# Optimization experiments

Measured on AMD Instinct MI355X. Metric: run time of the kernel, lower is better.

Reference implementation:

```python
import jax, jax.numpy as jnp
import numpy as np

KERNEL_MUL = 2.0
KERNEL_NUM = 5
FIX_SIGMA = None


def setup_inputs() -> dict:
    key = jax.random.key(0)
    k1, k2 = jax.random.split(key)
    source = jax.random.normal(k1, (4096, 512), dtype=jnp.float32)
    target = jax.random.normal(k2, (4096, 512), dtype=jnp.float32)
    return {"source": source, "target": target}


def reference(source, target):
    batch_size = source.shape[0]
    total = jnp.concatenate([source, target], axis=0)  # [N, D], N = n1 + n2
    n_samples = total.shape[0]

    # Pairwise squared L2 distances via Gram-matrix trick (same math as
    # the explicit NxNxD broadcast in the original, without materializing it).
    sq = jnp.sum(total * total, axis=1)               # [N]
    gram = total @ total.T                            # [N, N]
    l2 = sq[:, None] + sq[None, :] - 2.0 * gram       # [N, N]

    if FIX_SIGMA:
        bandwidth = jnp.asarray(FIX_SIGMA, dtype=l2.dtype)
    else:
        # torch used L2_distance.data -> no gradient through bandwidth
        bandwidth = jax.lax.stop_gradient(jnp.sum(l2)) / (n_samples ** 2 - n_samples)
    bandwidth = bandwidth / (KERNEL_MUL ** (KERNEL_NUM // 2))

    # Multi-bandwidth Gaussian kernel sum
    kernels = jnp.zeros_like(l2)
    for i in range(KERNEL_NUM):
        kernels = kernels + jnp.exp(-l2 / (bandwidth * (KERNEL_MUL ** i)))

    b = batch_size
    XX = kernels[:b, :b]
    YY = kernels[b:, b:]
    XY = kernels[:b, b:]
    YX = kernels[b:, :b]
    loss = jnp.mean(XX + YY - XY - YX)
    return loss
```

## Files before the change

### kernel.cpp

```cpp
#include <hip/hip_runtime.h>
#include <math.h>

typedef float f32x4 __attribute__((ext_vector_type(4)));
typedef int   i32x4 __attribute__((ext_vector_type(4)));
typedef signed char i8x8 __attribute__((ext_vector_type(8)));

#define NROWS 8192
#define NCOLS 512
#define BHALF 4096
#define NT    64
#define NBLK  2080
#define CSPART 256
#define QS    24.0f
#define INV_S2 (1.0f / (24.0f * 24.0f))

__global__ void k_conv(const float* __restrict__ src, const float* __restrict__ tgt,
                       signed char* __restrict__ bfrag, float* __restrict__ sq,
                       int* __restrict__ sqi, float* __restrict__ cspart) {
    __shared__ signed char ldsc[32][528];
    __shared__ float colp[4][NCOLS];
    int t = threadIdx.x, w = t >> 6, l = t & 63;
    int r0 = blockIdx.x * 32;
    float c0x=0.f,c0y=0.f,c0z=0.f,c0w=0.f, c1x=0.f,c1y=0.f,c1z=0.f,c1w=0.f;
    #pragma unroll
    for (int r = 0; r < 8; ++r) {
        int row = r0 + w * 8 + r;
        const float* base = (row < BHALF) ? (src + (size_t)row * NCOLS)
                                          : (tgt + (size_t)(row - BHALF) * NCOLS);
        float4 a = ((const float4*)base)[2 * l];
        float4 b = ((const float4*)base)[2 * l + 1];
        int q0 = (int)rintf(fminf(fmaxf(a.x * QS, -127.f), 127.f));
        int q1 = (int)rintf(fminf(fmaxf(a.y * QS, -127.f), 127.f));
        int q2 = (int)rintf(fminf(fmaxf(a.z * QS, -127.f), 127.f));
        int q3 = (int)rintf(fminf(fmaxf(a.w * QS, -127.f), 127.f));
        int q4 = (int)rintf(fminf(fmaxf(b.x * QS, -127.f), 127.f));
        int q5 = (int)rintf(fminf(fmaxf(b.y * QS, -127.f), 127.f));
        int q6 = (int)rintf(fminf(fmaxf(b.z * QS, -127.f), 127.f));
        int q7 = (int)rintf(fminf(fmaxf(b.w * QS, -127.f), 127.f));
        i8x8 v8;
        v8[0]=(signed char)q0; v8[1]=(signed char)q1; v8[2]=(signed char)q2; v8[3]=(signed char)q3;
        v8[4]=(signed char)q4; v8[5]=(signed char)q5; v8[6]=(signed char)q6; v8[7]=(signed char)q7;
        *(i8x8*)&ldsc[w * 8 + r][l * 8] = v8;
        float s = a.x*a.x + a.y*a.y + a.z*a.z + a.w*a.w
                + b.x*b.x + b.y*b.y + b.z*b.z + b.w*b.w;
        int si = q0*q0 + q1*q1 + q2*q2 + q3*q3 + q4*q4 + q5*q5 + q6*q6 + q7*q7;
        #pragma unroll
        for (int o = 32; o > 0; o >>= 1) {
            s  += __shfl_down(s, o);
            si += __shfl_down(si, o);
        }
        if (l == 0) { sq[row] = s; sqi[row] = si; }
        c0x += a.x; c0y += a.y; c0z += a.z; c0w += a.w;
        c1x += b.x; c1y += b.y; c1z += b.z; c1w += b.w;
    }
    colp[w][l*8+0] = c0x; colp[w][l*8+1] = c0y; colp[w][l*8+2] = c0z; colp[w][l*8+3] = c0w;
    colp[w][l*8+4] = c1x; colp[w][l*8+5] = c1y; colp[w][l*8+6] = c1z; colp[w][l*8+7] = c1w;
    __syncthreads();
    float s0 = colp[0][t] + colp[1][t] + colp[2][t] + colp[3][t];
    float s1 = colp[0][t+256] + colp[1][t+256] + colp[2][t+256] + colp[3][t+256];
    cspart[(size_t)blockIdx.x * NCOLS + t]       = s0;
    cspart[(size_t)blockIdx.x * NCOLS + t + 256] = s1;
    int rg0 = blockIdx.x * 2;
    #pragma unroll
    for (int c4 = 0; c4 < 4; ++c4) {
        int c = c4 * 256 + t;
        int g = c >> 9, sl = (c >> 4) & 31, lrr = c & 15;
        i32x4 v = *(const i32x4*)&ldsc[g * 16 + lrr][sl * 16];
        *(i32x4*)(bfrag + (size_t)(rg0 + g) * 8192 + sl * 256 + lrr * 16) = v;
    }
}

__global__ void k_bw(const float* __restrict__ sq, const float* __restrict__ cspart,
                     float* __restrict__ cvals) {
    __shared__ double red[1024];
    int t = threadIdx.x;
    double a = 0.0;
    #pragma unroll
    for (int i = 0; i < 8; ++i) a += (double)sq[t + i * 1024];
    red[t] = a; __syncthreads();
    for (int o = 512; o > 0; o >>= 1) { if (t < o) red[t] += red[t + o]; __syncthreads(); }
    double sT = red[0];
    __syncthreads();
    int c = t & 511, h = t >> 9;
    double d0 = 0.0, d1 = 0.0, d2 = 0.0, d3 = 0.0;
    int p0 = h * 128;
    #pragma unroll 8
    for (int p = 0; p < 128; p += 4) {
        d0 += (double)cspart[(size_t)(p0 + p + 0) * NCOLS + c];
        d1 += (double)cspart[(size_t)(p0 + p + 1) * NCOLS + c];
        d2 += (double)cspart[(size_t)(p0 + p + 2) * NCOLS + c];
        d3 += (double)cspart[(size_t)(p0 + p + 3) * NCOLS + c];
    }
    red[t] = (d0 + d1) + (d2 + d3);
    __syncthreads();
    double v = 0.0;
    if (t < 512) { double cs = red[t] + red[t + 512]; v = cs * cs; }
    __syncthreads();
    red[t] = v; __syncthreads();
    for (int o = 512; o > 0; o >>= 1) { if (t < o) red[t] += red[t + o]; __syncthreads(); }
    if (t == 0) {
        double G = red[0];
        double sum_l2 = 2.0 * (double)NROWS * sT - 2.0 * G;
        double denom = (double)NROWS * (double)NROWS - (double)NROWS;
        double bw = sum_l2 / denom / 4.0;
        const double L2E = 1.4426950408889634;
        double b = bw;
        #pragma unroll
        for (int k = 0; k < 5; ++k) { cvals[k] = (float)(L2E / b); b *= 2.0; }
    }
}

__global__ __launch_bounds__(256, 3)
void k_mmd(const signed char* __restrict__ bfrag, const int* __restrict__ sqi,
           const float* __restrict__ cvals, double* __restrict__ psum) {
    __shared__ float wred[4];

    int bid = blockIdx.x;
    int swz = (bid & 7) * (NBLK / 8) + (bid >> 3);
    int rem = swz;
    int I = 0;
    while (rem >= NT - I) { rem -= NT - I; ++I; }
    int J = I + rem;

    const int t  = threadIdx.x;
    const int w  = t >> 6;
    const int l  = t & 63;
    const int lr = l & 15;
    const int lk = l >> 4;

    const bool dsup = (I == J);
    int da, db;
    if (dsup) { da = (w == 2) ? 1 : 0; db = (w == 0) ? 0 : 1; }
    else      { da = w >> 1;           db = w & 1; }
    const int i_t = 2 * I + da, j_t = 2 * J + db;
    const int rowA0 = i_t * 64, rowB0 = j_t * 64;

    const int i_u = __builtin_amdgcn_readfirstlane(i_t);
    const int j_u = __builtin_amdgcn_readfirstlane(j_t);
    const signed char* bA = bfrag + (size_t)i_u * 32768;
    const signed char* bB = bfrag + (size_t)j_u * 32768;
    const int voff = lk * 256 + lr * 16;

    i32x4 acc[4][4] = {};
    #pragma unroll
    for (int kt = 0; kt < 8; ++kt) {
        i32x4 af[4], bf[4];
        #pragma unroll
        for (int m = 0; m < 4; ++m)
            af[m] = *(const i32x4*)(bA + m * 8192 + kt * 1024 + voff);
        #pragma unroll
        for (int n = 0; n < 4; ++n)
            bf[n] = *(const i32x4*)(bB + n * 8192 + kt * 1024 + voff);
        __builtin_amdgcn_s_setprio(1);
        #pragma unroll
        for (int m = 0; m < 4; ++m)
            #pragma unroll
            for (int n = 0; n < 4; ++n)
                acc[m][n] = __builtin_amdgcn_mfma_i32_16x16x64_i8(
                    af[m], bf[n], acc[m][n], 0, 0, 0);
        __builtin_amdgcn_s_setprio(0);
    }

    i32x4 sqa[4];
    #pragma unroll
    for (int m = 0; m < 4; ++m)
        sqa[m] = *(const i32x4*)&sqi[rowA0 + m * 16 + lk * 4];
    int sqb[4];
    #pragma unroll
    for (int n = 0; n < 4; ++n)
        sqb[n] = sqi[rowB0 + n * 16 + lr];
    float c4i = cvals[4] * INV_S2;

    const bool elem = dsup && ((w & 1) == 0);
    const float wb  = dsup ? 1.f : 2.f;
    const float sgn = ((rowA0 < BHALF) == (rowB0 < BHALF)) ? 1.f : -1.f;
    float local = 0.f;
    #pragma unroll
    for (int m = 0; m < 4; ++m)
        #pragma unroll
        for (int n = 0; n < 4; ++n)
            #pragma unroll
            for (int r = 0; r < 4; ++r) {
                int   d   = acc[m][n][r];
                int   l2i = sqa[m][r] + sqb[n] - 2 * d;
                float l2  = (float)l2i;
                float x  = exp2f(-l2 * c4i);
                float x2 = x * x;
                float x4 = x2 * x2;
                float x8 = x4 * x4;
                float e  = x + x2 + x4 + x8 + x8 * x8;
                if (elem) {
                    int gi = rowA0 + m * 16 + lk * 4 + r;
                    int gj = rowB0 + n * 16 + lr;
                    float wgt = (gj > gi) ? 2.f : ((gj == gi) ? 1.f : 0.f);
                    local += wgt * e;
                } else {
                    local += e;
                }
            }
    if (!elem) local *= wb * sgn;

    #pragma unroll
    for (int o = 32; o > 0; o >>= 1) local += __shfl_down(local, o);
    if (l == 0) wred[w] = local;
    __syncthreads();
    if (t == 0) {
        psum[blockIdx.x] = (double)((wred[0] + wred[1]) + (wred[2] + wred[3]));
    }
}

__global__ void k_final(const double* __restrict__ psum, float* __restrict__ out) {
    __shared__ double red[256];
    int t = threadIdx.x;
    double a = 0.0;
    for (int i = t; i < NBLK; i += 256) a += psum[i];
    red[t] = a; __syncthreads();
    for (int o = 128; o > 0; o >>= 1) { if (t < o) red[t] += red[t + o]; __syncthreads(); }
    if (t == 0) out[0] = (float)(red[0] * (1.0 / ((double)BHALF * (double)BHALF)));
}

extern "C" void kernel_launch(void* const* d_in, const int* in_sizes, int n_in,
                              void* d_out, int out_size, void* d_ws, size_t ws_size,
                              hipStream_t stream) {
    (void)in_sizes; (void)n_in; (void)out_size; (void)ws_size;
    const float* src = (const float*)d_in[0];
    const float* tgt = (const float*)d_in[1];
    float* out = (float*)d_out;
    char* ws = (char*)d_ws;
    signed char* bfrag = (signed char*)(ws);
    float*  sq     = (float*) (ws + 4194304);
    int*    sqi    = (int*)   (ws + 4194304 + 32768);
    float*  cspart = (float*) (ws + 4194304 + 65536);
    float*  cvals  = (float*) (ws + 4194304 + 65536 + 524288);
    double* psum   = (double*)(ws + 4194304 + 65536 + 524288 + 32);

    k_conv  <<<CSPART, 256, 0, stream>>>(src, tgt, bfrag, sq, sqi, cspart);
    k_bw    <<<1, 1024, 0, stream>>>(sq, cspart, cvals);
    k_mmd   <<<NBLK, 256, 0, stream>>>(bfrag, sqi, cvals, psum);
    k_final <<<1, 256, 0, stream>>>(psum, out);
}
```

Measured before the change: 64.98 us.

## Split bandwidth reduction across blocks and tune MMD tile mapping and exp math

The per-row float squared-norm reduction becomes a per-block double partial in the conversion kernel. The column-sum reduction moves out of the single-block bandwidth kernel into a new 8-block kernel, so the serial kernel does much less. In the MMD kernel, the linear while-loop that finds the tile index is replaced by a sqrt-based closed form, s_setprio is removed, launch bounds go from 3 to 4 blocks per SM, and exp2f becomes the hardware builtin with an FMA in the kernel sum. This adds one extra kernel launch, and the higher occupancy target may cause register spills.

Result: faster. 62.65 us (-3.6%).

```diff
diff --git a/kernel.cpp b/kernel.cpp
--- a/kernel.cpp
+++ b/kernel.cpp
@@ -15,13 +15,15 @@
 #define INV_S2 (1.0f / (24.0f * 24.0f))
 
 __global__ void k_conv(const float* __restrict__ src, const float* __restrict__ tgt,
-                       signed char* __restrict__ bfrag, float* __restrict__ sq,
-                       int* __restrict__ sqi, float* __restrict__ cspart) {
+                       signed char* __restrict__ bfrag, int* __restrict__ sqi,
+                       double* __restrict__ sqpart, float* __restrict__ cspart) {
     __shared__ signed char ldsc[32][528];
     __shared__ float colp[4][NCOLS];
+    __shared__ double dred[4];
     int t = threadIdx.x, w = t >> 6, l = t & 63;
     int r0 = blockIdx.x * 32;
     float c0x=0.f,c0y=0.f,c0z=0.f,c0w=0.f, c1x=0.f,c1y=0.f,c1z=0.f,c1w=0.f;
+    double facc = 0.0;
     #pragma unroll
     for (int r = 0; r < 8; ++r) {
         int row = r0 + w * 8 + r;
@@ -43,19 +45,21 @@
         *(i8x8*)&ldsc[w * 8 + r][l * 8] = v8;
         float s = a.x*a.x + a.y*a.y + a.z*a.z + a.w*a.w
                 + b.x*b.x + b.y*b.y + b.z*b.z + b.w*b.w;
+        facc += (double)s;
         int si = q0*q0 + q1*q1 + q2*q2 + q3*q3 + q4*q4 + q5*q5 + q6*q6 + q7*q7;
         #pragma unroll
-        for (int o = 32; o > 0; o >>= 1) {
-            s  += __shfl_down(s, o);
-            si += __shfl_down(si, o);
-        }
-        if (l == 0) { sq[row] = s; sqi[row] = si; }
+        for (int o = 32; o > 0; o >>= 1) si += __shfl_down(si, o);
+        if (l == 0) sqi[row] = si;
         c0x += a.x; c0y += a.y; c0z += a.z; c0w += a.w;
         c1x += b.x; c1y += b.y; c1z += b.z; c1w += b.w;
     }
+    #pragma unroll
+    for (int o = 32; o > 0; o >>= 1) facc += __shfl_down(facc, o);
+    if (l == 0) dred[w] = facc;
     colp[w][l*8+0] = c0x; colp[w][l*8+1] = c0y; colp[w][l*8+2] = c0z; colp[w][l*8+3] = c0w;
     colp[w][l*8+4] = c1x; colp[w][l*8+5] = c1y; colp[w][l*8+6] = c1z; colp[w][l*8+7] = c1w;
     __syncthreads();
+    if (t == 0) sqpart[blockIdx.x] = (dred[0] + dred[1]) + (dred[2] + dred[3]);
     float s0 = colp[0][t] + colp[1][t] + colp[2][t] + colp[3][t];
     float s1 = colp[0][t+256] + colp[1][t+256] + colp[2][t+256] + colp[3][t+256];
     cspart[(size_t)blockIdx.x * NCOLS + t]       = s0;
@@ -70,34 +74,33 @@
     }
 }
 
-__global__ void k_bw(const float* __restrict__ sq, const float* __restrict__ cspart,
+__global__ void k_red(const float* __restrict__ cspart, double* __restrict__ colsq) {
+    __shared__ double lred[4][64];
+    int b = blockIdx.x, t = threadIdx.x;
+    int c = b * 64 + (t & 63), q = t >> 6;
+    double a = 0.0;
+    #pragma unroll 4
+    for (int p = q * 64; p < q * 64 + 64; ++p)
+        a += (double)cspart[(size_t)p * NCOLS + c];
+    lred[q][t & 63] = a;
+    __syncthreads();
+    if (t < 64) {
+        double s = (lred[0][t] + lred[1][t]) + (lred[2][t] + lred[3][t]);
+        colsq[b * 64 + t] = s * s;
+    }
+}
+
+__global__ void k_bw(const double* __restrict__ sqpart, const double* __restrict__ colsq,
                      float* __restrict__ cvals) {
-    __shared__ double red[1024];
+    __shared__ double red[512];
     int t = threadIdx.x;
-    double a = 0.0;
-    #pragma unroll
-    for (int i = 0; i < 8; ++i) a += (double)sq[t + i * 1024];
-    red[t] = a; __syncthreads();
-    for (int o = 512; o > 0; o >>= 1) { if (t < o) red[t] += red[t + o]; __syncthreads(); }
+    red[t] = (t < CSPART) ? sqpart[t] : 0.0;
+    __syncthreads();
+    for (int o = 256; o > 0; o >>= 1) { if (t < o) red[t] += red[t + o]; __syncthreads(); }
     double sT = red[0];
     __syncthreads();
-    int c = t & 511, h = t >> 9;
-    double d0 = 0.0, d1 = 0.0, d2 = 0.0, d3 = 0.0;
-    int p0 = h * 128;
-    #pragma unroll 8
-    for (int p = 0; p < 128; p += 4) {
-        d0 += (double)cspart[(size_t)(p0 + p + 0) * NCOLS + c];
-        d1 += (double)cspart[(size_t)(p0 + p + 1) * NCOLS + c];
-        d2 += (double)cspart[(size_t)(p0 + p + 2) * NCOLS + c];
-        d3 += (double)cspart[(size_t)(p0 + p + 3) * NCOLS + c];
-    }
-    red[t] = (d0 + d1) + (d2 + d3);
-    __syncthreads();
-    double v = 0.0;
-    if (t < 512) { double cs = red[t] + red[t + 512]; v = cs * cs; }
-    __syncthreads();
-    red[t] = v; __syncthreads();
-    for (int o = 512; o > 0; o >>= 1) { if (t < o) red[t] += red[t + o]; __syncthreads(); }
+    red[t] = colsq[t]; __syncthreads();
+    for (int o = 256; o > 0; o >>= 1) { if (t < o) red[t] += red[t + o]; __syncthreads(); }
     if (t == 0) {
         double G = red[0];
         double sum_l2 = 2.0 * (double)NROWS * sT - 2.0 * G;
@@ -110,17 +113,19 @@
     }
 }
 
-__global__ __launch_bounds__(256, 3)
+__global__ __launch_bounds__(256, 4)
 void k_mmd(const signed char* __restrict__ bfrag, const int* __restrict__ sqi,
            const float* __restrict__ cvals, double* __restrict__ psum) {
     __shared__ float wred[4];
 
     int bid = blockIdx.x;
     int swz = (bid & 7) * (NBLK / 8) + (bid >> 3);
-    int rem = swz;
-    int I = 0;
-    while (rem >= NT - I) { rem -= NT - I; ++I; }
-    int J = I + rem;
+    int v = NBLK - 1 - swz;
+    int k = (int)((sqrtf(8.f * (float)v + 1.f) - 1.f) * 0.5f);
+    while ((k + 1) * (k + 2) / 2 <= v) ++k;
+    while (k * (k + 1) / 2 > v) --k;
+    int I = NT - 1 - k;
+    int J = NT - 1 - (v - k * (k + 1) / 2);
 
     const int t  = threadIdx.x;
     const int w  = t >> 6;
@@ -151,14 +156,12 @@
         #pragma unroll
         for (int n = 0; n < 4; ++n)
             bf[n] = *(const i32x4*)(bB + n * 8192 + kt * 1024 + voff);
-        __builtin_amdgcn_s_setprio(1);
         #pragma unroll
         for (int m = 0; m < 4; ++m)
             #pragma unroll
             for (int n = 0; n < 4; ++n)
                 acc[m][n] = __builtin_amdgcn_mfma_i32_16x16x64_i8(
                     af[m], bf[n], acc[m][n], 0, 0, 0);
-        __builtin_amdgcn_s_setprio(0);
     }
 
     i32x4 sqa[4];
@@ -184,11 +187,11 @@
                 int   d   = acc[m][n][r];
                 int   l2i = sqa[m][r] + sqb[n] - 2 * d;
                 float l2  = (float)l2i;
-                float x  = exp2f(-l2 * c4i);
+                float x  = __builtin_amdgcn_exp2f(-l2 * c4i);
                 float x2 = x * x;
                 float x4 = x2 * x2;
                 float x8 = x4 * x4;
-                float e  = x + x2 + x4 + x8 + x8 * x8;
+                float e  = fmaf(x8, x8, x8) + ((x + x2) + x4);
                 if (elem) {
                     int gi = rowA0 + m * 16 + lk * 4 + r;
                     int gj = rowB0 + n * 16 + lr;
@@ -210,12 +213,13 @@
 }
 
 __global__ void k_final(const double* __restrict__ psum, float* __restrict__ out) {
-    __shared__ double red[256];
+    __shared__ double red[512];
     int t = threadIdx.x;
     double a = 0.0;
-    for (int i = t; i < NBLK; i += 256) a += psum[i];
+    #pragma unroll
+    for (int i = t; i < NBLK; i += 512) a += psum[i];
     red[t] = a; __syncthreads();
-    for (int o = 128; o > 0; o >>= 1) { if (t < o) red[t] += red[t + o]; __syncthreads(); }
+    for (int o = 256; o > 0; o >>= 1) { if (t < o) red[t] += red[t + o]; __syncthreads(); }
     if (t == 0) out[0] = (float)(red[0] * (1.0 / ((double)BHALF * (double)BHALF)));
 }
 
@@ -228,14 +232,16 @@
     float* out = (float*)d_out;
     char* ws = (char*)d_ws;
     signed char* bfrag = (signed char*)(ws);
-    float*  sq     = (float*) (ws + 4194304);
-    int*    sqi    = (int*)   (ws + 4194304 + 32768);
-    float*  cspart = (float*) (ws + 4194304 + 65536);
-    float*  cvals  = (float*) (ws + 4194304 + 65536 + 524288);
-    double* psum   = (double*)(ws + 4194304 + 65536 + 524288 + 32);
-
-    k_conv  <<<CSPART, 256, 0, stream>>>(src, tgt, bfrag, sq, sqi, cspart);
-    k_bw    <<<1, 1024, 0, stream>>>(sq, cspart, cvals);
+    int*    sqi    = (int*)   (ws + 4194304);
+    float*  cspart = (float*) (ws + 4227072);
+    float*  cvals  = (float*) (ws + 4751360);
+    double* colsq  = (double*)(ws + 4751392);
+    double* sqpart = (double*)(ws + 4755488);
+    double* psum   = (double*)(ws + 4757536);
+
+    k_conv  <<<CSPART, 256, 0, stream>>>(src, tgt, bfrag, sqi, sqpart, cspart);
+    k_red   <<<8, 256, 0, stream>>>(cspart, colsq);
+    k_bw    <<<1, 512, 0, stream>>>(sqpart, colsq, cvals);
     k_mmd   <<<NBLK, 256, 0, stream>>>(bfrag, sqi, cvals, psum);
-    k_final <<<1, 256, 0, stream>>>(psum, out);
-}
+    k_final <<<1, 512, 0, stream>>>(psum, out);
+}
```
